# Performance work log

Hardware: AMD Instinct MI355X
Metric: run time of the kernel (lower is better)

The kernel has to match this reference:

```python
import jax, jax.numpy as jnp
import numpy as np

I, H, B, T = 17, 128, 32768, 19

def setup_inputs() -> dict:
    key = jax.random.key(0)
    ks = jax.random.split(key, 7)
    s = 1.0 / np.sqrt(H)  # PyTorch LSTMCell/Linear init scale
    u = lambda k, shape: jax.random.uniform(k, shape, jnp.float32, -s, s)
    return {
        "x": jax.random.normal(ks[0], (B, T, I), jnp.float32),
        "W_ih": u(ks[1], (4 * H, I)),
        "W_hh": u(ks[2], (4 * H, H)),
        "b_ih": u(ks[3], (4 * H,)),
        "b_hh": u(ks[4], (4 * H,)),
        "W_out": u(ks[5], (I, H)),
        "b_out": u(ks[6], (I,)),
    }

def reference(x, W_ih, W_hh, b_ih, b_hh, W_out, b_out):
    B_, T_, _ = x.shape
    Hh = W_hh.shape[1]
    # Precompute input projections for all timesteps in one GEMM: [B,T,4H]
    x_proj = jnp.einsum('bti,gi->btg', x, W_ih) + b_ih + b_hh

    def step(carry, xp_t):
        h, c = carry
        gates = xp_t + h @ W_hh.T            # [B,4H]
        i_g, f_g, g_g, o_g = jnp.split(gates, 4, axis=-1)
        c = jax.nn.sigmoid(f_g) * c + jax.nn.sigmoid(i_g) * jnp.tanh(g_g)
        h = jax.nn.sigmoid(o_g) * jnp.tanh(c)
        y = h @ W_out.T + b_out              # [B,I]
        return (h, c), y

    h0 = jnp.zeros((B_, Hh), x.dtype)
    c0 = jnp.zeros((B_, Hh), x.dtype)
    _, ys = jax.lax.scan(step, (h0, c0), jnp.swapaxes(x_proj, 0, 1))  # ys: [T,B,I]
    return jnp.swapaxes(ys, 0, 1)  # [B,T,I]
```

## Files before the change

kernel.cpp:

```cpp
#include <hip/hip_runtime.h>

#define I_DIM 17
#define H_DIM 128
#define T_DIM 19
#define B_DIM 32768
#define M_ROWS 64
#define NTHR 1024
#define XI (T_DIM * I_DIM)

typedef __bf16 bf16x8 __attribute__((ext_vector_type(8)));
typedef float f32x4 __attribute__((ext_vector_type(4)));

union FragU { bf16x8 v; unsigned short s[8]; uint4 u; };

__device__ __forceinline__ unsigned short f2bf(float f) {
    union { float f; unsigned u; } x; x.f = f;
    unsigned r = x.u + 0x7fffu + ((x.u >> 16) & 1u);
    return (unsigned short)(r >> 16);
}
__device__ __forceinline__ float sigm(float v) {
    float e = __builtin_amdgcn_exp2f(-1.4426950408889634f * v);
    return __builtin_amdgcn_rcpf(1.0f + e);
}
__device__ __forceinline__ float tanh_(float v) {
    float e = __builtin_amdgcn_exp2f(-2.8853900817779268f * v);
    return 2.0f * __builtin_amdgcn_rcpf(1.0f + e) - 1.0f;
}

#define LDS_H   131072
#define LDS_WOF 147456
#define LDS_X   155648
#define LDS_TOT 160768

__global__ __launch_bounds__(NTHR) void flowlstm(
    const float* __restrict__ x, const float* __restrict__ W_ih,
    const float* __restrict__ W_hh, const float* __restrict__ b_ih,
    const float* __restrict__ b_hh, const float* __restrict__ W_out,
    const float* __restrict__ b_out, float* __restrict__ out)
{
    __shared__ __align__(16) unsigned char smem[LDS_TOT];
    unsigned char* WhF = smem;
    unsigned char* Hl  = smem + LDS_H;
    unsigned char* WoF = smem + LDS_WOF;
    unsigned char* Xl  = smem + LDS_X;

    const int tid  = threadIdx.x;
    const int w    = tid >> 6;
    const int lane = tid & 63;
    const int l15  = lane & 15;
    const int q    = lane >> 4;
    const int wg   = w & 3;
    const int half = (w >> 2) & 1;
    const int mth  = w >> 3;
    const int b0   = blockIdx.x * M_ROWS;

    #pragma unroll
    for (int i = 0; i < 8; ++i) {
        int lr = tid + i * NTHR;
        int ln = lr & 63, f = lr >> 6;
        int g = f & 3, kk = (f >> 2) & 3, hh = (f >> 4) & 1, wgs = f >> 5;
        int n  = g * 128 + wgs * 32 + hh * 16 + (ln & 15);
        int kb = kk * 32 + (ln >> 4) * 8;
        const float* s = W_hh + n * H_DIM + kb;
        FragU fu;
        #pragma unroll
        for (int e = 0; e < 8; ++e) fu.s[e] = f2bf(s[e]);
        *(uint4*)(WhF + lr * 16) = fu.u;
    }
    if (tid < 512) {
        int ln = tid & 63, f = tid >> 6;
        int kk = f & 3, nt = f >> 2;
        int o  = nt * 16 + (ln & 15);
        int kb = kk * 32 + (ln >> 4) * 8;
        FragU fu;
        #pragma unroll
        for (int e = 0; e < 8; ++e)
            fu.s[e] = (o < I_DIM) ? f2bf(W_out[o * H_DIM + kb + e]) : (unsigned short)0;
        *(uint4*)(WoF + tid * 16) = fu.u;
    }
    #pragma unroll
    for (int i = 0; i < 4; ++i) ((unsigned*)Hl)[tid + i * NTHR] = 0u;
    for (int e = tid; e < 1280; e += NTHR) ((unsigned*)Xl)[e] = 0u;

    bf16x8 wih[4];
    #pragma unroll
    for (int g = 0; g < 4; ++g) {
        int n = g * 128 + wg * 32 + half * 16 + l15;
        FragU fu;
        #pragma unroll
        for (int e = 0; e < 8; ++e) {
            int k = q * 8 + e;
            fu.s[e] = (k < I_DIM) ? f2bf(W_ih[n * I_DIM + k]) : (unsigned short)0;
        }
        wih[g] = fu.v;
    }
    float bias[4];
    #pragma unroll
    for (int g = 0; g < 4; ++g) {
        int col = g * 128 + wg * 32 + half * 16 + l15;
        bias[g] = b_ih[col] + b_hh[col];
    }
    const int ymt = w >> 1, ynt = w & 1;
    const float ybo = (ynt == 0) ? b_out[l15] : b_out[16];

    const int  f1   = tid;
    const int  row1 = f1 / I_DIM, k1 = f1 - row1 * I_DIM;
    const bool v2   = (tid < M_ROWS * I_DIM - NTHR);
    const int  f2   = tid + NTHR;
    const int  row2 = v2 ? (f2 / I_DIM) : 0;
    const int  k2   = v2 ? (f2 - (f2 / I_DIM) * I_DIM) : 0;
    const size_t gb1 = (size_t)(b0 + row1) * XI + k1;
    const size_t gb2 = (size_t)(b0 + row2) * XI + k2;
    const int lo1 = row1 * 80 + k1 * 2;
    const int lo2 = row2 * 80 + k2 * 2;

    __syncthreads();
    *(unsigned short*)(Xl + lo1) = f2bf(x[gb1]);
    if (v2) *(unsigned short*)(Xl + lo2) = f2bf(x[gb2]);

    float cst[8];
    #pragma unroll
    for (int i = 0; i < 8; ++i) cst[i] = 0.0f;

    __syncthreads();

    float xr1 = 0.f, xr2 = 0.f;
    for (int t = 0; t < T_DIM; ++t) {
        if (t + 1 < T_DIM) {
            xr1 = x[gb1 + (size_t)(t + 1) * I_DIM];
            if (v2) xr2 = x[gb2 + (size_t)(t + 1) * I_DIM];
        }
        if (t > 0 && w < 8) {
            f32x4 ya = {0.f, 0.f, 0.f, 0.f};
            int arow = ymt * 16 + l15;
            #pragma unroll
            for (int kk = 0; kk < 4; ++kk) {
                unsigned aoff = (unsigned)(arow * 256 + ((((kk << 6) | (q << 4))) ^ ((arow & 7) << 4)));
                bf16x8 a = *(const bf16x8*)(Hl + aoff);
                bf16x8 b = *(const bf16x8*)(WoF + (((ynt * 4 + kk)) << 10) + lane * 16);
                ya = __builtin_amdgcn_mfma_f32_16x16x32_bf16(a, b, ya, 0, 0, 0);
            }
            if (ynt == 0 || l15 == 0) {
                int col = ynt * 16 + l15;
                #pragma unroll
                for (int r = 0; r < 4; ++r) {
                    int row = ymt * 16 + q * 4 + r;
                    out[((size_t)(b0 + row) * T_DIM + (t - 1)) * I_DIM + col] = ya[r] + ybo;
                }
            }
        }
        f32x4 acc[2][4];
        #pragma unroll
        for (int mtl = 0; mtl < 2; ++mtl)
            #pragma unroll
            for (int g = 0; g < 4; ++g)
                acc[mtl][g] = (f32x4){bias[g], bias[g], bias[g], bias[g]};

        #pragma unroll
        for (int kk = 0; kk < 4; ++kk) {
            bf16x8 bf[4];
            unsigned fb = ((unsigned)(((wg * 2 + half) * 4 + kk) * 4) << 10) + lane * 16;
            #pragma unroll
            for (int g = 0; g < 4; ++g)
                bf[g] = *(const bf16x8*)(WhF + fb + (g << 10));
            #pragma unroll
            for (int mtl = 0; mtl < 2; ++mtl) {
                int arow = (mth * 2 + mtl) * 16 + l15;
                unsigned aoff = (unsigned)(arow * 256 + ((((kk << 6) | (q << 4))) ^ ((arow & 7) << 4)));
                bf16x8 a = *(const bf16x8*)(Hl + aoff);
                #pragma unroll
                for (int g = 0; g < 4; ++g)
                    acc[mtl][g] = __builtin_amdgcn_mfma_f32_16x16x32_bf16(a, bf[g], acc[mtl][g], 0, 0, 0);
            }
        }
        #pragma unroll
        for (int mtl = 0; mtl < 2; ++mtl) {
            int arow = (mth * 2 + mtl) * 16 + l15;
            bf16x8 a = *(const bf16x8*)(Xl + arow * 80 + q * 16);
            #pragma unroll
            for (int g = 0; g < 4; ++g)
                acc[mtl][g] = __builtin_amdgcn_mfma_f32_16x16x32_bf16(a, wih[g], acc[mtl][g], 0, 0, 0);
        }
        unsigned hvp[4];
        #pragma unroll
        for (int mtl = 0; mtl < 2; ++mtl) {
            unsigned short hs[4];
            #pragma unroll
            for (int r = 0; r < 4; ++r) {
                float ig = acc[mtl][0][r], fg = acc[mtl][1][r];
                float gg = acc[mtl][2][r], og = acc[mtl][3][r];
                float c  = sigm(fg) * cst[mtl * 4 + r] + sigm(ig) * tanh_(gg);
                cst[mtl * 4 + r] = c;
                hs[r] = f2bf(sigm(og) * tanh_(c));
            }
            hvp[mtl * 2 + 0] = (unsigned)hs[0] | ((unsigned)hs[1] << 16);
            hvp[mtl * 2 + 1] = (unsigned)hs[2] | ((unsigned)hs[3] << 16);
        }
        __syncthreads();
        {
            int col2 = (wg * 32 + half * 16 + l15) * 2;
            #pragma unroll
            for (int mtl = 0; mtl < 2; ++mtl)
                #pragma unroll
                for (int r = 0; r < 4; ++r) {
                    int row = (mth * 2 + mtl) * 16 + q * 4 + r;
                    unsigned off = (unsigned)(row * 256 + (col2 ^ ((row & 7) << 4)));
                    unsigned vv = hvp[mtl * 2 + (r >> 1)];
                    *(unsigned short*)(Hl + off) = (unsigned short)((r & 1) ? (vv >> 16) : vv);
                }
        }
        if (t + 1 < T_DIM) {
            *(unsigned short*)(Xl + lo1) = f2bf(xr1);
            if (v2) *(unsigned short*)(Xl + lo2) = f2bf(xr2);
        }
        __syncthreads();
    }
    if (w < 8) {
        f32x4 ya = {0.f, 0.f, 0.f, 0.f};
        int arow = ymt * 16 + l15;
        #pragma unroll
        for (int kk = 0; kk < 4; ++kk) {
            unsigned aoff = (unsigned)(arow * 256 + ((((kk << 6) | (q << 4))) ^ ((arow & 7) << 4)));
            bf16x8 a = *(const bf16x8*)(Hl + aoff);
            bf16x8 b = *(const bf16x8*)(WoF + (((ynt * 4 + kk)) << 10) + lane * 16);
            ya = __builtin_amdgcn_mfma_f32_16x16x32_bf16(a, b, ya, 0, 0, 0);
        }
        if (ynt == 0 || l15 == 0) {
            int col = ynt * 16 + l15;
            #pragma unroll
            for (int r = 0; r < 4; ++r) {
                int row = ymt * 16 + q * 4 + r;
                out[((size_t)(b0 + row) * T_DIM + (T_DIM - 1)) * I_DIM + col] = ya[r] + ybo;
            }
        }
    }
}

extern "C" void kernel_launch(void* const* d_in, const int* in_sizes, int n_in,
                              void* d_out, int out_size, void* d_ws, size_t ws_size,
                              hipStream_t stream) {
    const float* x     = (const float*)d_in[0];
    const float* W_ih  = (const float*)d_in[1];
    const float* W_hh  = (const float*)d_in[2];
    const float* b_ih  = (const float*)d_in[3];
    const float* b_hh  = (const float*)d_in[4];
    const float* W_out = (const float*)d_in[5];
    const float* b_out = (const float*)d_in[6];
    float* out = (float*)d_out;

    dim3 grid(B_DIM / M_ROWS), block(NTHR);
    flowlstm<<<grid, block, 0, stream>>>(x, W_ih, W_hh, b_ih, b_hh, W_out, b_out, out);
}
```

Measured before the change: 171.3 us.

## Hold W_hh fragments in registers and process small row tiles sequentially per block

Blocks shrink to 512 threads, each handling four sequential 16-row batch tiles, and W_hh bf16 fragments now sit in registers instead of a 128KB LDS copy. LDS use falls to about 46KB, so several blocks can share a CU and the per-step LDS weight loads go away. The gate math is merged into fewer reciprocals, and the recurrent MFMA is skipped at t=0. In exchange, register pressure rises (64 VGPRs of weights under a 4-blocks launch bound), and each block processes the 19-step recurrence four times, once per tile.

```diff
diff --git a/kernel.cpp b/kernel.cpp
--- a/kernel.cpp
+++ b/kernel.cpp
@@ -4,233 +4,191 @@
 #define H_DIM 128
 #define T_DIM 19
 #define B_DIM 32768
-#define M_ROWS 64
-#define NTHR 1024
+#define M_ROWS 16
+#define TILES 4
+#define NTHR 512
+#define GRID (B_DIM / (M_ROWS * TILES))
 #define XI (T_DIM * I_DIM)
 
 typedef __bf16 bf16x8 __attribute__((ext_vector_type(8)));
 typedef float f32x4 __attribute__((ext_vector_type(4)));
 
 union FragU { bf16x8 v; unsigned short s[8]; uint4 u; };
+
+#define OFF_WOF 32768
+#define OFF_H   40960
+#define OFF_X   45056
+#define LDS_TOT 47104
 
 __device__ __forceinline__ unsigned short f2bf(float f) {
     union { float f; unsigned u; } x; x.f = f;
     unsigned r = x.u + 0x7fffu + ((x.u >> 16) & 1u);
     return (unsigned short)(r >> 16);
 }
-__device__ __forceinline__ float sigm(float v) {
-    float e = __builtin_amdgcn_exp2f(-1.4426950408889634f * v);
-    return __builtin_amdgcn_rcpf(1.0f + e);
-}
-__device__ __forceinline__ float tanh_(float v) {
-    float e = __builtin_amdgcn_exp2f(-2.8853900817779268f * v);
-    return 2.0f * __builtin_amdgcn_rcpf(1.0f + e) - 1.0f;
-}
-
-#define LDS_H   131072
-#define LDS_WOF 147456
-#define LDS_X   155648
-#define LDS_TOT 160768
-
-__global__ __launch_bounds__(NTHR) void flowlstm(
+
+#define K1 1.4426950408889634f
+#define K2 2.8853900817779268f
+
+__global__ __launch_bounds__(NTHR, 4) void flowlstm(
     const float* __restrict__ x, const float* __restrict__ W_ih,
     const float* __restrict__ W_hh, const float* __restrict__ b_ih,
     const float* __restrict__ b_hh, const float* __restrict__ W_out,
     const float* __restrict__ b_out, float* __restrict__ out)
 {
     __shared__ __align__(16) unsigned char smem[LDS_TOT];
-    unsigned char* WhF = smem;
-    unsigned char* Hl  = smem + LDS_H;
-    unsigned char* WoF = smem + LDS_WOF;
-    unsigned char* Xl  = smem + LDS_X;
-
-    const int tid  = threadIdx.x;
-    const int w    = tid >> 6;
-    const int lane = tid & 63;
-    const int l15  = lane & 15;
-    const int q    = lane >> 4;
-    const int wg   = w & 3;
-    const int half = (w >> 2) & 1;
-    const int mth  = w >> 3;
-    const int b0   = blockIdx.x * M_ROWS;
-
-    #pragma unroll
-    for (int i = 0; i < 8; ++i) {
-        int lr = tid + i * NTHR;
-        int ln = lr & 63, f = lr >> 6;
-        int g = f & 3, kk = (f >> 2) & 3, hh = (f >> 4) & 1, wgs = f >> 5;
-        int n  = g * 128 + wgs * 32 + hh * 16 + (ln & 15);
-        int kb = kk * 32 + (ln >> 4) * 8;
-        const float* s = W_hh + n * H_DIM + kb;
+    const int tid = threadIdx.x;
+    const int w = tid >> 6, lane = tid & 63, l15 = lane & 15, q = lane >> 4;
+    const int wg = w & 3, half = w >> 2;
+
+    #pragma unroll
+    for (int i = 0; i < 4; ++i) {
+        int s = tid + i * NTHR;
+        int ln = s & 63, f = s >> 6;
+        int g = f & 3, hf = (f >> 2) & 1, wgs = f >> 3;
+        int n = g * H_DIM + wgs * 32 + hf * 16 + (ln & 15);
+        int kb = (ln >> 4) * 8;
         FragU fu;
         #pragma unroll
-        for (int e = 0; e < 8; ++e) fu.s[e] = f2bf(s[e]);
-        *(uint4*)(WhF + lr * 16) = fu.u;
-    }
-    if (tid < 512) {
+        for (int e = 0; e < 8; ++e)
+            fu.s[e] = (kb + e < I_DIM) ? f2bf(W_ih[n * I_DIM + kb + e]) : (unsigned short)0;
+        *(uint4*)(smem + f * 1024 + ln * 16) = fu.u;
+    }
+    {
         int ln = tid & 63, f = tid >> 6;
         int kk = f & 3, nt = f >> 2;
-        int o  = nt * 16 + (ln & 15);
+        int o = nt * 16 + (ln & 15);
         int kb = kk * 32 + (ln >> 4) * 8;
         FragU fu;
         #pragma unroll
         for (int e = 0; e < 8; ++e)
             fu.s[e] = (o < I_DIM) ? f2bf(W_out[o * H_DIM + kb + e]) : (unsigned short)0;
-        *(uint4*)(WoF + tid * 16) = fu.u;
-    }
-    #pragma unroll
-    for (int i = 0; i < 4; ++i) ((unsigned*)Hl)[tid + i * NTHR] = 0u;
-    for (int e = tid; e < 1280; e += NTHR) ((unsigned*)Xl)[e] = 0u;
-
-    bf16x8 wih[4];
+        *(uint4*)(smem + OFF_WOF + f * 1024 + ln * 16) = fu.u;
+    }
+    ((unsigned*)(smem + OFF_X))[tid] = 0u;
+
+    bf16x8 whh[4][4];
+    #pragma unroll
+    for (int kk = 0; kk < 4; ++kk)
+        #pragma unroll
+        for (int g = 0; g < 4; ++g) {
+            int n = g * H_DIM + wg * 32 + half * 16 + l15;
+            const float* s = W_hh + n * H_DIM + kk * 32 + q * 8;
+            FragU fu;
+            #pragma unroll
+            for (int e = 0; e < 8; ++e) fu.s[e] = f2bf(s[e]);
+            whh[kk][g] = fu.v;
+        }
+    float bias[4];
     #pragma unroll
     for (int g = 0; g < 4; ++g) {
-        int n = g * 128 + wg * 32 + half * 16 + l15;
-        FragU fu;
-        #pragma unroll
-        for (int e = 0; e < 8; ++e) {
-            int k = q * 8 + e;
-            fu.s[e] = (k < I_DIM) ? f2bf(W_ih[n * I_DIM + k]) : (unsigned short)0;
+        int col = g * H_DIM + wg * 32 + half * 16 + l15;
+        bias[g] = b_ih[col] + b_hh[col];
+    }
+    const unsigned xr7 = (unsigned)((l15 & 7) << 4);
+    unsigned aoff[4], woff[4];
+    #pragma unroll
+    for (int kk = 0; kk < 4; ++kk)
+        aoff[kk] = (unsigned)(OFF_H + l15 * 256 + (((kk * 64) | (q * 16)) ^ xr7));
+    #pragma unroll
+    for (int r = 0; r < 4; ++r) {
+        int row = q * 4 + r;
+        woff[r] = (unsigned)(OFF_H + row * 256 +
+                             (((wg * 32 + half * 16 + l15) * 2) ^ ((row & 7) << 4)));
+    }
+    const unsigned xaoff = (unsigned)(OFF_X + l15 * 80 + q * 16);
+    const unsigned wifb  = (unsigned)(((wg * 2 + half) * 4) * 1024 + lane * 16);
+    const float ybo = (w == 0) ? b_out[l15] : b_out[16];
+
+    const bool xv = tid < M_ROWS * I_DIM;
+    const int xrow = tid / I_DIM;
+    const int xk = tid - xrow * I_DIM;
+    const unsigned xlo = (unsigned)(OFF_X + xrow * 80 + xk * 2);
+
+    __syncthreads();
+
+    #pragma unroll 1
+    for (int tile = 0; tile < TILES; ++tile) {
+        const int b0 = blockIdx.x * (M_ROWS * TILES) + tile * M_ROWS;
+        const float* xp = x + (size_t)(b0 + xrow) * XI + xk;
+        float cst[4] = {0.f, 0.f, 0.f, 0.f};
+        if (xv) *(unsigned short*)(smem + xlo) = f2bf(xp[0]);
+        __syncthreads();
+        float xr1 = 0.f;
+        #pragma unroll 1
+        for (int t = 0; t < T_DIM; ++t) {
+            if (xv && t + 1 < T_DIM) xr1 = xp[(size_t)(t + 1) * I_DIM];
+            if (t > 0 && w < 2) {
+                f32x4 ya = {0.f, 0.f, 0.f, 0.f};
+                #pragma unroll
+                for (int kk = 0; kk < 4; ++kk) {
+                    bf16x8 a = *(const bf16x8*)(smem + aoff[kk]);
+                    bf16x8 b = *(const bf16x8*)(smem + OFF_WOF + (w * 4 + kk) * 1024 + lane * 16);
+                    ya = __builtin_amdgcn_mfma_f32_16x16x32_bf16(a, b, ya, 0, 0, 0);
+                }
+                int col = w * 16 + l15;
+                if (col < I_DIM) {
+                    #pragma unroll
+                    for (int r = 0; r < 4; ++r)
+                        out[((size_t)(b0 + q * 4 + r) * T_DIM + (t - 1)) * I_DIM + col] = ya[r] + ybo;
+                }
+            }
+            f32x4 acc[4];
+            #pragma unroll
+            for (int g = 0; g < 4; ++g) acc[g] = (f32x4){bias[g], bias[g], bias[g], bias[g]};
+            {
+                bf16x8 a = *(const bf16x8*)(smem + xaoff);
+                #pragma unroll
+                for (int g = 0; g < 4; ++g) {
+                    bf16x8 b = *(const bf16x8*)(smem + wifb + g * 1024);
+                    acc[g] = __builtin_amdgcn_mfma_f32_16x16x32_bf16(a, b, acc[g], 0, 0, 0);
+                }
+            }
+            if (t > 0) {
+                #pragma unroll
+                for (int kk = 0; kk < 4; ++kk) {
+                    bf16x8 a = *(const bf16x8*)(smem + aoff[kk]);
+                    #pragma unroll
+                    for (int g = 0; g < 4; ++g)
+                        acc[g] = __builtin_amdgcn_mfma_f32_16x16x32_bf16(a, whh[kk][g], acc[g], 0, 0, 0);
+                }
+            }
+            unsigned short hs[4];
+            #pragma unroll
+            for (int r = 0; r < 4; ++r) {
+                float ig = acc[0][r], fg = acc[1][r], gg = acc[2][r], og = acc[3][r];
+                float ui = __builtin_amdgcn_exp2f(-K1 * ig);
+                float uf = __builtin_amdgcn_exp2f(-K1 * fg);
+                float vg = __builtin_amdgcn_exp2f(-K2 * gg);
+                float uo = __builtin_amdgcn_exp2f(-K1 * og);
+                float A = 1.f + ui, F = 1.f + uf, G = 1.f + vg;
+                float AG = A * G;
+                float num = cst[r] * AG + (1.f - vg) * F;
+                float c = num * __builtin_amdgcn_rcpf(F * AG);
+                cst[r] = c;
+                float vc = __builtin_amdgcn_exp2f(-K2 * c);
+                float h = (1.f - vc) * __builtin_amdgcn_rcpf((1.f + uo) * (1.f + vc));
+                hs[r] = f2bf(h);
+            }
+            __syncthreads();
+            #pragma unroll
+            for (int r = 0; r < 4; ++r)
+                *(unsigned short*)(smem + woff[r]) = hs[r];
+            if (xv && t + 1 < T_DIM) *(unsigned short*)(smem + xlo) = f2bf(xr1);
+            __syncthreads();
         }
-        wih[g] = fu.v;
-    }
-    float bias[4];
-    #pragma unroll
-    for (int g = 0; g < 4; ++g) {
-        int col = g * 128 + wg * 32 + half * 16 + l15;
-        bias[g] = b_ih[col] + b_hh[col];
-    }
-    const int ymt = w >> 1, ynt = w & 1;
-    const float ybo = (ynt == 0) ? b_out[l15] : b_out[16];
-
-    const int  f1   = tid;
-    const int  row1 = f1 / I_DIM, k1 = f1 - row1 * I_DIM;
-    const bool v2   = (tid < M_ROWS * I_DIM - NTHR);
-    const int  f2   = tid + NTHR;
-    const int  row2 = v2 ? (f2 / I_DIM) : 0;
-    const int  k2   = v2 ? (f2 - (f2 / I_DIM) * I_DIM) : 0;
-    const size_t gb1 = (size_t)(b0 + row1) * XI + k1;
-    const size_t gb2 = (size_t)(b0 + row2) * XI + k2;
-    const int lo1 = row1 * 80 + k1 * 2;
-    const int lo2 = row2 * 80 + k2 * 2;
-
-    __syncthreads();
-    *(unsigned short*)(Xl + lo1) = f2bf(x[gb1]);
-    if (v2) *(unsigned short*)(Xl + lo2) = f2bf(x[gb2]);
-
-    float cst[8];
-    #pragma unroll
-    for (int i = 0; i < 8; ++i) cst[i] = 0.0f;
-
-    __syncthreads();
-
-    float xr1 = 0.f, xr2 = 0.f;
-    for (int t = 0; t < T_DIM; ++t) {
-        if (t + 1 < T_DIM) {
-            xr1 = x[gb1 + (size_t)(t + 1) * I_DIM];
-            if (v2) xr2 = x[gb2 + (size_t)(t + 1) * I_DIM];
-        }
-        if (t > 0 && w < 8) {
+        if (w < 2) {
             f32x4 ya = {0.f, 0.f, 0.f, 0.f};
-            int arow = ymt * 16 + l15;
             #pragma unroll
             for (int kk = 0; kk < 4; ++kk) {
-                unsigned aoff = (unsigned)(arow * 256 + ((((kk << 6) | (q << 4))) ^ ((arow & 7) << 4)));
-                bf16x8 a = *(const bf16x8*)(Hl + aoff);
-                bf16x8 b = *(const bf16x8*)(WoF + (((ynt * 4 + kk)) << 10) + lane * 16);
+                bf16x8 a = *(const bf16x8*)(smem + aoff[kk]);
+                bf16x8 b = *(const bf16x8*)(smem + OFF_WOF + (w * 4 + kk) * 1024 + lane * 16);
                 ya = __builtin_amdgcn_mfma_f32_16x16x32_bf16(a, b, ya, 0, 0, 0);
             }
-            if (ynt == 0 || l15 == 0) {
-                int col = ynt * 16 + l15;
-                #pragma unroll
-                for (int r = 0; r < 4; ++r) {
-                    int row = ymt * 16 + q * 4 + r;
-                    out[((size_t)(b0 + row) * T_DIM + (t - 1)) * I_DIM + col] = ya[r] + ybo;
-                }
-            }
-        }
-        f32x4 acc[2][4];
-        #pragma unroll
-        for (int mtl = 0; mtl < 2; ++mtl)
-            #pragma unroll
-            for (int g = 0; g < 4; ++g)
-                acc[mtl][g] = (f32x4){bias[g], bias[g], bias[g], bias[g]};
-
-        #pragma unroll
-        for (int kk = 0; kk < 4; ++kk) {
-            bf16x8 bf[4];
-            unsigned fb = ((unsigned)(((wg * 2 + half) * 4 + kk) * 4) << 10) + lane * 16;
-            #pragma unroll
-            for (int g = 0; g < 4; ++g)
-                bf[g] = *(const bf16x8*)(WhF + fb + (g << 10));
-            #pragma unroll
-            for (int mtl = 0; mtl < 2; ++mtl) {
-                int arow = (mth * 2 + mtl) * 16 + l15;
-                unsigned aoff = (unsigned)(arow * 256 + ((((kk << 6) | (q << 4))) ^ ((arow & 7) << 4)));
-                bf16x8 a = *(const bf16x8*)(Hl + aoff);
-                #pragma unroll
-                for (int g = 0; g < 4; ++g)
-                    acc[mtl][g] = __builtin_amdgcn_mfma_f32_16x16x32_bf16(a, bf[g], acc[mtl][g], 0, 0, 0);
-            }
-        }
-        #pragma unroll
-        for (int mtl = 0; mtl < 2; ++mtl) {
-            int arow = (mth * 2 + mtl) * 16 + l15;
-            bf16x8 a = *(const bf16x8*)(Xl + arow * 80 + q * 16);
-            #pragma unroll
-            for (int g = 0; g < 4; ++g)
-                acc[mtl][g] = __builtin_amdgcn_mfma_f32_16x16x32_bf16(a, wih[g], acc[mtl][g], 0, 0, 0);
-        }
-        unsigned hvp[4];
-        #pragma unroll
-        for (int mtl = 0; mtl < 2; ++mtl) {
-            unsigned short hs[4];
-            #pragma unroll
-            for (int r = 0; r < 4; ++r) {
-                float ig = acc[mtl][0][r], fg = acc[mtl][1][r];
-                float gg = acc[mtl][2][r], og = acc[mtl][3][r];
-                float c  = sigm(fg) * cst[mtl * 4 + r] + sigm(ig) * tanh_(gg);
-                cst[mtl * 4 + r] = c;
-                hs[r] = f2bf(sigm(og) * tanh_(c));
-            }
-            hvp[mtl * 2 + 0] = (unsigned)hs[0] | ((unsigned)hs[1] << 16);
-            hvp[mtl * 2 + 1] = (unsigned)hs[2] | ((unsigned)hs[3] << 16);
-        }
-        __syncthreads();
-        {
-            int col2 = (wg * 32 + half * 16 + l15) * 2;
-            #pragma unroll
-            for (int mtl = 0; mtl < 2; ++mtl)
-                #pragma unroll
-                for (int r = 0; r < 4; ++r) {
-                    int row = (mth * 2 + mtl) * 16 + q * 4 + r;
-                    unsigned off = (unsigned)(row * 256 + (col2 ^ ((row & 7) << 4)));
-                    unsigned vv = hvp[mtl * 2 + (r >> 1)];
-                    *(unsigned short*)(Hl + off) = (unsigned short)((r & 1) ? (vv >> 16) : vv);
-                }
-        }
-        if (t + 1 < T_DIM) {
-            *(unsigned short*)(Xl + lo1) = f2bf(xr1);
-            if (v2) *(unsigned short*)(Xl + lo2) = f2bf(xr2);
-        }
-        __syncthreads();
-    }
-    if (w < 8) {
-        f32x4 ya = {0.f, 0.f, 0.f, 0.f};
-        int arow = ymt * 16 + l15;
-        #pragma unroll
-        for (int kk = 0; kk < 4; ++kk) {
-            unsigned aoff = (unsigned)(arow * 256 + ((((kk << 6) | (q << 4))) ^ ((arow & 7) << 4)));
-            bf16x8 a = *(const bf16x8*)(Hl + aoff);
-            bf16x8 b = *(const bf16x8*)(WoF + (((ynt * 4 + kk)) << 10) + lane * 16);
-            ya = __builtin_amdgcn_mfma_f32_16x16x32_bf16(a, b, ya, 0, 0, 0);
-        }
-        if (ynt == 0 || l15 == 0) {
-            int col = ynt * 16 + l15;
-            #pragma unroll
-            for (int r = 0; r < 4; ++r) {
-                int row = ymt * 16 + q * 4 + r;
-                out[((size_t)(b0 + row) * T_DIM + (T_DIM - 1)) * I_DIM + col] = ya[r] + ybo;
+            int col = w * 16 + l15;
+            if (col < I_DIM) {
+                #pragma unroll
+                for (int r = 0; r < 4; ++r)
+                    out[((size_t)(b0 + q * 4 + r) * T_DIM + (T_DIM - 1)) * I_DIM + col] = ya[r] + ybo;
             }
         }
     }
@@ -248,6 +206,6 @@
     const float* b_out = (const float*)d_in[6];
     float* out = (float*)d_out;
 
-    dim3 grid(B_DIM / M_ROWS), block(NTHR);
+    dim3 grid(GRID), block(NTHR);
     flowlstm<<<grid, block, 0, stream>>>(x, W_ih, W_hh, b_ih, b_hh, W_out, b_out, out);
 }
```

Result: slower. 196.1 us (+14.5%).
